# Kernel tuning notes

Hardware: AMD Instinct MI355X
Metric: run time of the kernel (lower is better)

Reference implementation:

```python
import jax, jax.numpy as jnp
import numpy as np

N_NODES = 65536   # N
D_HID   = 128     # D (hidden)
N_GROUPS = 16384  # G portfolios
GROUP_LEN = 64    # lines per portfolio (port_len entries)
N_LINES = N_GROUPS * GROUP_LEN  # L
BATCH = 16384     # B samples


def setup_inputs() -> dict:
    key = jax.random.key(0)
    k = jax.random.split(key, 5)
    H = jax.random.normal(k[0], (N_NODES, D_HID), dtype=jnp.float32)
    port_w_signed_flat = jax.random.normal(k[1], (N_LINES,), dtype=jnp.float32)
    anchor_idx = jax.random.randint(k[2], (BATCH,), 0, N_NODES, dtype=jnp.int32)
    pf_gid = jax.random.randint(k[3], (BATCH,), 0, N_GROUPS, dtype=jnp.int32)
    port_nodes_flat = jax.random.randint(k[4], (N_LINES,), 0, N_NODES, dtype=jnp.int32)
    port_len = jnp.full((N_GROUPS,), GROUP_LEN, dtype=jnp.int32)
    return {
        'H': H,
        'port_w_signed_flat': port_w_signed_flat,
        'anchor_idx': anchor_idx,
        'pf_gid': pf_gid,
        'port_nodes_flat': port_nodes_flat,
        'port_len': port_len,
    }


def reference(H, port_w_signed_flat, anchor_idx, pf_gid, port_nodes_flat, port_len):
    """Faithful, vectorized port of compute_samplewise_portfolio_vectors_loo.

    Ragged segment-weighted mean per portfolio group, with strict leave-one-out
    correction for each sample's anchor node, followed by L2 normalization.
    Returns (V_abs, V_sgn), each [B, D].
    """
    N, D = H.shape
    G = port_len.shape[0]
    L = port_nodes_flat.shape[0]

    # gid per flat line: repeat_interleave(arange(G), lens)
    gid_lines = jnp.repeat(jnp.arange(G, dtype=jnp.int32), port_len,
                           total_repeat_length=L)

    w_abs = jnp.abs(port_w_signed_flat)
    Hl = H[port_nodes_flat]                                  # [L, D] gather
    S_abs = jax.ops.segment_sum(w_abs[:, None] * Hl, gid_lines, num_segments=G)
    W_abs = jax.ops.segment_sum(w_abs, gid_lines, num_segments=G)
    W_sgn = jax.ops.segment_sum(port_w_signed_flat, gid_lines, num_segments=G)

    valid = (pf_gid >= 0) & (pf_gid < G)
    g = jnp.clip(pf_gid, 0, G - 1)

    # Leave-one-out self-weight: sum of w over lines where (gid==g_i, node==anchor_i).
    # Vectorized join via a sorted composite int32 key (G*N < 2^31 by construction).
    keys_l = gid_lines * N + port_nodes_flat                 # [L]
    keys_s = g * N + anchor_idx                              # [B]
    order = jnp.argsort(keys_l)
    sk = keys_l[order]
    zero1 = jnp.zeros((1,), H.dtype)
    ca = jnp.concatenate([zero1, jnp.cumsum(w_abs[order])])
    cs = jnp.concatenate([zero1, jnp.cumsum(port_w_signed_flat[order])])
    lo = jnp.searchsorted(sk, keys_s, side='left')
    hi = jnp.searchsorted(sk, keys_s, side='right')
    self_w_abs = ca[hi] - ca[lo]                             # [B]
    self_w_sgn = cs[hi] - cs[lo]                             # [B]

    Ha = H[anchor_idx]                                       # [B, D]
    denom = jnp.maximum(W_abs[g] - self_w_abs, 1e-12)        # clamp_min
    V_abs = (S_abs[g] - self_w_abs[:, None] * Ha) / denom[:, None]
    V_sgn = ((W_sgn[g] - self_w_sgn) / denom)[:, None] * V_abs

    V_abs = jnp.where(valid[:, None], V_abs, jnp.zeros((), H.dtype))
    V_sgn = jnp.where(valid[:, None], V_sgn, jnp.zeros((), H.dtype))

    # torch F.normalize: x / clamp(||x||, min=eps)
    na = jnp.linalg.norm(V_abs, axis=1, keepdims=True)
    V_abs = V_abs / jnp.maximum(na, 1e-6)
    ns = jnp.linalg.norm(V_sgn, axis=1, keepdims=True)
    V_sgn = jnp.where(ns > 0, V_sgn / jnp.maximum(ns, 1e-6), V_sgn)
    return V_abs, V_sgn
```

## Files before the change

### kernel.cpp

```cpp
#include <hip/hip_runtime.h>
#include <hip/hip_bf16.h>


#define DDIM 128

__device__ inline unsigned bf_rne(float x) {
    unsigned u = __float_as_uint(x);
    return (u + 0x7FFFu + ((u >> 16) & 1u)) >> 16;
}

__device__ inline void unpack2(unsigned d, float& lo, float& hi) {
    lo = __uint_as_float(d << 16);
    hi = __uint_as_float(d & 0xFFFF0000u);
}

__global__ __launch_bounds__(1024) void init_kernel(
    const float4* __restrict__ H4, uint2* __restrict__ Hb, int n4, int N,
    const int* __restrict__ plen, int* __restrict__ offs, int G,
    const int* __restrict__ pf_gid, int* __restrict__ used, int B, int nconv) {
    const int t = threadIdx.x;
    const int bb = blockIdx.x;
    if (bb < nconv) {
        const int i = bb * 1024 + t;
        if (i < n4) {
            const float4 v = H4[i];
            uint2 o;
            o.x = bf_rne(v.x) | (bf_rne(v.y) << 16);
            o.y = bf_rne(v.z) | (bf_rne(v.w) << 16);
            const int n = i >> 5;
            const int j = i & 31;
            const int cc = j >> 2;
            Hb[(size_t)cc * ((size_t)N * 4) + n * 4 + (j & 3)] = o;
        }
        return;
    }
    if (bb == nconv) {
        for (int i = t; i < G; i += 1024) used[i] = 0;
        __syncthreads();
        for (int i = t; i < B; i += 1024) {
            const int g = pf_gid[i];
            if (g >= 0 && g < G) used[g] = 1;
        }
        return;
    }
    __shared__ int part[1024];
    const int chunk = (G + 1023) >> 10;
    const int lo = min(t * chunk, G);
    const int hi = min(lo + chunk, G);
    int s = 0;
    for (int i = lo; i < hi; ++i) s += plen[i];
    part[t] = s;
    __syncthreads();
    #pragma unroll
    for (int ofs = 1; ofs < 1024; ofs <<= 1) {
        int v = (t >= ofs) ? part[t - ofs] : 0;
        __syncthreads();
        part[t] += v;
        __syncthreads();
    }
    int run = part[t] - s;
    for (int i = lo; i < hi; ++i) { offs[i] = run; run += plen[i]; }
}

__global__ __launch_bounds__(256) void group_sums(
    const unsigned short* __restrict__ Hp,
    const float* __restrict__ pw, const int* __restrict__ pn,
    const int* __restrict__ plen, const int* __restrict__ offs,
    const int* __restrict__ used,
    float* __restrict__ Sabs, float* __restrict__ Wag,
    float* __restrict__ Wsg, int G, int N) {
    const int b = blockIdx.x;
    const int c = b & 7;
    const int g = (b >> 3) * 4 + (threadIdx.x >> 6);
    if (g >= G) return;
    if (!used[g]) return;
    const int lane = threadIdx.x & 63;
    const int q = lane >> 2;
    const int s = lane & 3;
    const unsigned short* plane = Hp + (size_t)c * ((size_t)N * 16);

    const int off = offs[g];
    const int len = plen[g];

    float acc0 = 0.f, acc1 = 0.f, acc2 = 0.f, acc3 = 0.f;
    float laWa = 0.f, laWs = 0.f;

    for (int base = 0; base < len; base += 64) {
        float wl = 0.f;
        int nl = 0;
        if (base + lane < len) {
            wl = pw[off + base + lane];
            nl = pn[off + base + lane];
        }
        if (c == 0) { laWa += fabsf(wl); laWs += wl; }

        #pragma unroll
        for (int it = 0; it < 4; ++it) {
            const int src = it * 16 + q;
            const float ww = fabsf(__shfl(wl, src));
            const int row = __shfl(nl, src);
            const uint2 h = *(const uint2*)(plane + (size_t)row * 16 + s * 4);
            float f0, f1, f2, f3;
            unpack2(h.x, f0, f1);
            unpack2(h.y, f2, f3);
            acc0 = fmaf(ww, f0, acc0);
            acc1 = fmaf(ww, f1, acc1);
            acc2 = fmaf(ww, f2, acc2);
            acc3 = fmaf(ww, f3, acc3);
        }
    }

    #pragma unroll
    for (int m = 4; m < 64; m <<= 1) {
        acc0 += __shfl_xor(acc0, m);
        acc1 += __shfl_xor(acc1, m);
        acc2 += __shfl_xor(acc2, m);
        acc3 += __shfl_xor(acc3, m);
    }
    if (lane < 4) {
        float4* dst = (float4*)(Sabs + (size_t)g * DDIM + c * 16 + 4 * lane);
        *dst = make_float4(acc0, acc1, acc2, acc3);
    }
    if (c == 0) {
        #pragma unroll
        for (int m = 32; m; m >>= 1) {
            laWa += __shfl_xor(laWa, m);
            laWs += __shfl_xor(laWs, m);
        }
        if (lane == 0) { Wag[g] = laWa; Wsg[g] = laWs; }
    }
}

__global__ __launch_bounds__(256) void per_sample(
    const float* __restrict__ H,
    const float* __restrict__ pw, const int* __restrict__ pn,
    const int* __restrict__ plen, const int* __restrict__ offs,
    const float* __restrict__ Sabs, const float* __restrict__ Wag,
    const float* __restrict__ Wsg,
    const int* __restrict__ anchor_idx, const int* __restrict__ pf_gid,
    float* __restrict__ out, int B, int G) {
    const int b = blockIdx.x * (blockDim.x >> 6) + (threadIdx.x >> 6);
    const int lane = threadIdx.x & 63;
    if (b >= B) return;

    float2* outA = (float2*)(out + (size_t)b * DDIM);
    float2* outS = (float2*)(out + ((size_t)B + b) * DDIM);

    const int g = pf_gid[b];
    if (!(g >= 0 && g < G)) {
        const float2 z = make_float2(0.f, 0.f);
        outA[lane] = z;
        outS[lane] = z;
        return;
    }

    const int anchor = anchor_idx[b];
    const int off = offs[g];
    const int len = plen[g];

    float selfa = 0.f, selfs = 0.f;
    for (int base = 0; base < len; base += 64) {
        const int jmax = min(64, len - base);
        if (lane < jmax) {
            const float w = pw[off + base + lane];
            const int n = pn[off + base + lane];
            if (n == anchor) { selfa += fabsf(w); selfs += w; }
        }
    }
    #pragma unroll
    for (int m = 32; m; m >>= 1) {
        selfa += __shfl_xor(selfa, m);
        selfs += __shfl_xor(selfs, m);
    }

    const float Wa = Wag[g];
    const float Wsn = Wsg[g];
    const float2 S = ((const float2*)(Sabs + (size_t)g * DDIM))[lane];
    const float2 hv = ((const float2*)(H + (size_t)anchor * DDIM))[lane];

    const float denom = fmaxf(Wa - selfa, 1e-12f);
    float2 v;
    v.x = (S.x - selfa * hv.x) / denom;
    v.y = (S.y - selfa * hv.y) / denom;
    const float scale = (Wsn - selfs) / denom;

    float n2 = v.x * v.x + v.y * v.y;
    #pragma unroll
    for (int m = 32; m; m >>= 1) n2 += __shfl_xor(n2, m);
    const float na = sqrtf(n2);

    const float invA = 1.0f / fmaxf(na, 1e-6f);
    const float ns = fabsf(scale) * na;
    const float sgnscale = (ns > 0.f) ? (scale / fmaxf(ns, 1e-6f)) : scale;

    outA[lane] = make_float2(v.x * invA, v.y * invA);
    outS[lane] = make_float2(v.x * sgnscale, v.y * sgnscale);
}

__global__ __launch_bounds__(1024) void scan_only(
    const int* __restrict__ len, int* __restrict__ offs, int G) {
    __shared__ int part[1024];
    const int t = threadIdx.x;
    const int chunk = (G + 1023) >> 10;
    const int lo = min(t * chunk, G);
    const int hi = min(lo + chunk, G);
    int s = 0;
    for (int i = lo; i < hi; ++i) s += len[i];
    part[t] = s;
    __syncthreads();
    #pragma unroll
    for (int ofs = 1; ofs < 1024; ofs <<= 1) {
        int v = (t >= ofs) ? part[t - ofs] : 0;
        __syncthreads();
        part[t] += v;
        __syncthreads();
    }
    int run = part[t] - s;
    for (int i = lo; i < hi; ++i) { offs[i] = run; run += len[i]; }
}

__global__ __launch_bounds__(256) void pf_loo_f32(
    const float* __restrict__ H, const float* __restrict__ pw,
    const int* __restrict__ anchor_idx, const int* __restrict__ pf_gid,
    const int* __restrict__ pn, const int* __restrict__ plen,
    const int* __restrict__ offs, float* __restrict__ out, int B, int G) {
    const int b = blockIdx.x * (blockDim.x >> 6) + (threadIdx.x >> 6);
    const int lane = threadIdx.x & 63;
    const int half = lane >> 5;
    const int qlane = lane & 31;
    if (b >= B) return;
    float4* outA = (float4*)(out + (size_t)b * DDIM);
    float4* outS = (float4*)(out + ((size_t)B + b) * DDIM);
    const int gid = pf_gid[b];
    if (!(gid >= 0 && gid < G)) {
        float4 z = make_float4(0.f, 0.f, 0.f, 0.f);
        if (half == 0) { outA[qlane] = z; outS[qlane] = z; }
        return;
    }
    const int anchor = anchor_idx[b];
    const int off = offs[gid];
    const int len = plen[gid];
    float4 acc = make_float4(0.f, 0.f, 0.f, 0.f);
    float laWa = 0.f, laWs = 0.f, laSa = 0.f, laSs = 0.f;
    for (int base = 0; base < len; base += 64) {
        const int jmax = min(64, len - base);
        float wl = 0.f;
        int nl = -1;
        if (lane < jmax) { wl = pw[off + base + lane]; nl = pn[off + base + lane]; }
        const float wla = fabsf(wl);
        laWa += wla; laWs += wl;
        if (nl == anchor) { laSa += wla; laSs += wl; }
        #pragma unroll 8
        for (int jj = 0; jj < 64; jj += 2) {
            const float ww = fabsf(__shfl(wl, jj + half));
            const int row = __shfl(nl, jj + half);
            const float4 h = ((const float4*)(H + (size_t)row * DDIM))[qlane];
            acc.x = fmaf(ww, h.x, acc.x);
            acc.y = fmaf(ww, h.y, acc.y);
            acc.z = fmaf(ww, h.z, acc.z);
            acc.w = fmaf(ww, h.w, acc.w);
        }
    }
    #pragma unroll
    for (int m = 32; m; m >>= 1) {
        laWa += __shfl_xor(laWa, m);
        laWs += __shfl_xor(laWs, m);
        laSa += __shfl_xor(laSa, m);
        laSs += __shfl_xor(laSs, m);
    }
    acc.x += __shfl_xor(acc.x, 32);
    acc.y += __shfl_xor(acc.y, 32);
    acc.z += __shfl_xor(acc.z, 32);
    acc.w += __shfl_xor(acc.w, 32);
    const float denom = fmaxf(laWa - laSa, 1e-12f);
    const float4 hv = ((const float4*)(H + (size_t)anchor * DDIM))[qlane];
    float4 v;
    v.x = (acc.x - laSa * hv.x) / denom;
    v.y = (acc.y - laSa * hv.y) / denom;
    v.z = (acc.z - laSa * hv.z) / denom;
    v.w = (acc.w - laSa * hv.w) / denom;
    const float scale = (laWs - laSs) / denom;
    float n2 = v.x * v.x + v.y * v.y + v.z * v.z + v.w * v.w;
    #pragma unroll
    for (int m = 32; m; m >>= 1) n2 += __shfl_xor(n2, m);
    n2 *= 0.5f;
    const float na = sqrtf(n2);
    const float invA = 1.0f / fmaxf(na, 1e-6f);
    const float ns = fabsf(scale) * na;
    const float sgnscale = (ns > 0.f) ? (scale / fmaxf(ns, 1e-6f)) : scale;
    const float sc = half ? sgnscale : invA;
    float4 res = make_float4(v.x * sc, v.y * sc, v.z * sc, v.w * sc);
    float4* dst = half ? outS : outA;
    dst[qlane] = res;
}

extern "C" void kernel_launch(void* const* d_in, const int* in_sizes, int n_in,
                              void* d_out, int out_size, void* d_ws, size_t ws_size,
                              hipStream_t stream) {
    const float* H      = (const float*)d_in[0];
    const float* pw     = (const float*)d_in[1];
    const int* anchor   = (const int*)d_in[2];
    const int* gid      = (const int*)d_in[3];
    const int* pn       = (const int*)d_in[4];
    const int* plen     = (const int*)d_in[5];
    float* out          = (float*)d_out;

    const int B = in_sizes[2];
    const int G = in_sizes[5];
    const int ND = in_sizes[0];
    const int N  = ND / DDIM;
    const size_t hb_bytes = (size_t)ND * 2;
    const size_t sabs_bytes = (size_t)G * DDIM * 4;
    const size_t need = hb_bytes + sabs_bytes + (size_t)G * 4 * 4;

    if (ws_size >= need) {
        char* p = (char*)d_ws;
        unsigned short* Hb = (unsigned short*)p;        p += hb_bytes;
        float* Sabs        = (float*)p;                 p += sabs_bytes;
        int* offsp         = (int*)p;                   p += (size_t)G * 4;
        int* usedp         = (int*)p;                   p += (size_t)G * 4;
        float* Wag         = (float*)p;                 p += (size_t)G * 4;
        float* Wsg         = (float*)p;

        const int n4 = ND / 4;
        const int nconv = (n4 + 1023) / 1024;
        init_kernel<<<nconv + 2, 1024, 0, stream>>>(
            (const float4*)H, (uint2*)Hb, n4, N, plen, offsp, G, gid, usedp, B, nconv);

        const int gblocks = ((G + 3) / 4) * 8;
        group_sums<<<gblocks, 256, 0, stream>>>(Hb, pw, pn, plen, offsp, usedp,
                                                Sabs, Wag, Wsg, G, N);

        const int sblocks = (B + 3) / 4;
        per_sample<<<sblocks, 256, 0, stream>>>(H, pw, pn, plen, offsp, Sabs,
                                                Wag, Wsg, anchor, gid, out, B, G);
    } else {
        int* offsp = (int*)d_ws;
        scan_only<<<1, 1024, 0, stream>>>(plen, offsp, G);
        const int blocks = (B + 3) / 4;
        pf_loo_f32<<<blocks, 256, 0, stream>>>(H, pw, anchor, gid, pn, plen,
                                               offsp, out, B, G);
    }
}
```

Before: 159.7 us.

## Widen bf16 H planes to 64B and stage gathered rows via global_load_lds

Changes the bf16 copy of H from eight 16-element planes to four 32-element planes, so each gathered row segment is 64 bytes instead of 32. group_sums now gathers those segments straight into LDS with global_load_lds 16-byte transfers and then reads them back for the weighted accumulation. Each block covers 8 groups across 4 planes, and every wave now also accumulates the weight sums. per_sample reads the anchor row from the bf16 planes instead of the fp32 H, which lowers its precision. The aim is fewer, wider random gathers at the cost of LDS staging and explicit waitcnt synchronisation.

```diff
diff --git a/kernel.cpp b/kernel.cpp
--- a/kernel.cpp
+++ b/kernel.cpp
@@ -29,8 +29,9 @@
             o.y = bf_rne(v.z) | (bf_rne(v.w) << 16);
             const int n = i >> 5;
             const int j = i & 31;
-            const int cc = j >> 2;
-            Hb[(size_t)cc * ((size_t)N * 4) + n * 4 + (j & 3)] = o;
+            const int p = j >> 3;
+            const int k = j & 7;
+            Hb[(size_t)p * ((size_t)N * 8) + (size_t)n * 8 + k] = o;
         }
         return;
     }
@@ -70,39 +71,56 @@
     float* __restrict__ Sabs, float* __restrict__ Wag,
     float* __restrict__ Wsg, int G, int N) {
     const int b = blockIdx.x;
-    const int c = b & 7;
-    const int g = (b >> 3) * 4 + (threadIdx.x >> 6);
+    const int slot = b & 7;
+    const int p = slot & 3;
+    const int wid = threadIdx.x >> 6;
+    const int g = (b >> 3) * 8 + (slot >> 2) * 4 + wid;
     if (g >= G) return;
     if (!used[g]) return;
     const int lane = threadIdx.x & 63;
-    const int q = lane >> 2;
-    const int s = lane & 3;
-    const unsigned short* plane = Hp + (size_t)c * ((size_t)N * 16);
-
+
+    __shared__ unsigned char tile[4][4096];
+
+    const unsigned short* plane = Hp + (size_t)p * ((size_t)N * 32);
     const int off = offs[g];
     const int len = plen[g];
 
+    const int sg = lane & 3;
+    const int s8 = lane & 7;
     float acc0 = 0.f, acc1 = 0.f, acc2 = 0.f, acc3 = 0.f;
     float laWa = 0.f, laWs = 0.f;
 
     for (int base = 0; base < len; base += 64) {
+        asm volatile("s_waitcnt lgkmcnt(0)" ::: "memory");
+
         float wl = 0.f;
         int nl = 0;
         if (base + lane < len) {
             wl = pw[off + base + lane];
             nl = pn[off + base + lane];
         }
-        if (c == 0) { laWa += fabsf(wl); laWs += wl; }
+        laWa += fabsf(wl);
+        laWs += wl;
 
         #pragma unroll
         for (int it = 0; it < 4; ++it) {
-            const int src = it * 16 + q;
-            const float ww = fabsf(__shfl(wl, src));
-            const int row = __shfl(nl, src);
-            const uint2 h = *(const uint2*)(plane + (size_t)row * 16 + s * 4);
+            const int row = __shfl(nl, it * 16 + (lane >> 2));
+            const unsigned short* gp = plane + (size_t)row * 32 + sg * 8;
+            __builtin_amdgcn_global_load_lds(
+                (const __attribute__((address_space(1))) unsigned int*)gp,
+                (__attribute__((address_space(3))) unsigned int*)&tile[wid][it * 1024],
+                16, 0, 0);
+        }
+        asm volatile("s_waitcnt vmcnt(0)" ::: "memory");
+
+        #pragma unroll
+        for (int j = 0; j < 8; ++j) {
+            const int row = j * 8 + (lane >> 3);
+            const float ww = fabsf(__shfl(wl, row));
+            const uint2 hv = *(const uint2*)&tile[wid][row * 64 + s8 * 8];
             float f0, f1, f2, f3;
-            unpack2(h.x, f0, f1);
-            unpack2(h.y, f2, f3);
+            unpack2(hv.x, f0, f1);
+            unpack2(hv.y, f2, f3);
             acc0 = fmaf(ww, f0, acc0);
             acc1 = fmaf(ww, f1, acc1);
             acc2 = fmaf(ww, f2, acc2);
@@ -111,17 +129,17 @@
     }
 
     #pragma unroll
-    for (int m = 4; m < 64; m <<= 1) {
+    for (int m = 8; m < 64; m <<= 1) {
         acc0 += __shfl_xor(acc0, m);
         acc1 += __shfl_xor(acc1, m);
         acc2 += __shfl_xor(acc2, m);
         acc3 += __shfl_xor(acc3, m);
     }
-    if (lane < 4) {
-        float4* dst = (float4*)(Sabs + (size_t)g * DDIM + c * 16 + 4 * lane);
+    if (lane < 8) {
+        float4* dst = (float4*)(Sabs + (size_t)g * DDIM + p * 32 + 4 * lane);
         *dst = make_float4(acc0, acc1, acc2, acc3);
     }
-    if (c == 0) {
+    if (p == 0) {
         #pragma unroll
         for (int m = 32; m; m >>= 1) {
             laWa += __shfl_xor(laWa, m);
@@ -132,13 +150,13 @@
 }
 
 __global__ __launch_bounds__(256) void per_sample(
-    const float* __restrict__ H,
+    const unsigned short* __restrict__ Hp,
     const float* __restrict__ pw, const int* __restrict__ pn,
     const int* __restrict__ plen, const int* __restrict__ offs,
     const float* __restrict__ Sabs, const float* __restrict__ Wag,
     const float* __restrict__ Wsg,
     const int* __restrict__ anchor_idx, const int* __restrict__ pf_gid,
-    float* __restrict__ out, int B, int G) {
+    float* __restrict__ out, int B, int G, int N) {
     const int b = blockIdx.x * (blockDim.x >> 6) + (threadIdx.x >> 6);
     const int lane = threadIdx.x & 63;
     if (b >= B) return;
@@ -176,12 +194,15 @@
     const float Wa = Wag[g];
     const float Wsn = Wsg[g];
     const float2 S = ((const float2*)(Sabs + (size_t)g * DDIM))[lane];
-    const float2 hv = ((const float2*)(H + (size_t)anchor * DDIM))[lane];
+    const unsigned hb = *(const unsigned*)(Hp + (size_t)(lane >> 4) * ((size_t)N * 32)
+                                              + (size_t)anchor * 32 + (lane & 15) * 2);
+    float h0, h1;
+    unpack2(hb, h0, h1);
 
     const float denom = fmaxf(Wa - selfa, 1e-12f);
     float2 v;
-    v.x = (S.x - selfa * hv.x) / denom;
-    v.y = (S.y - selfa * hv.y) / denom;
+    v.x = (S.x - selfa * h0) / denom;
+    v.y = (S.y - selfa * h1) / denom;
     const float scale = (Wsn - selfs) / denom;
 
     float n2 = v.x * v.x + v.y * v.y;
@@ -327,13 +348,13 @@
         init_kernel<<<nconv + 2, 1024, 0, stream>>>(
             (const float4*)H, (uint2*)Hb, n4, N, plen, offsp, G, gid, usedp, B, nconv);
 
-        const int gblocks = ((G + 3) / 4) * 8;
+        const int gblocks = ((G + 7) / 8) * 8;
         group_sums<<<gblocks, 256, 0, stream>>>(Hb, pw, pn, plen, offsp, usedp,
                                                 Sabs, Wag, Wsg, G, N);
 
         const int sblocks = (B + 3) / 4;
-        per_sample<<<sblocks, 256, 0, stream>>>(H, pw, pn, plen, offsp, Sabs,
-                                                Wag, Wsg, anchor, gid, out, B, G);
+        per_sample<<<sblocks, 256, 0, stream>>>(Hb, pw, pn, plen, offsp, Sabs,
+                                                Wag, Wsg, anchor, gid, out, B, G, N);
     } else {
         int* offsp = (int*)d_ws;
         scan_only<<<1, 1024, 0, stream>>>(plen, offsp, G);
```

After: 146.3 us. 1.09x faster.
